# Performance work log

Hardware: AMD Instinct MI355X
Metric: run time of the kernel (lower is better)

## Reference

```python
import jax, jax.numpy as jnp
import numpy as np

B, L, D = 2, 4096, 1024
H, DK, DV = 4, 256, 256
CONV_K, FIR_S, FIR_L = 4, 3, 31
CHUNK = 32
EPS = 1e-5


def l2norm(x):
    return x * jax.lax.rsqrt(jnp.sum(x * x, -1, keepdims=True) + 1e-6)


def causal_dwconv(x, w):
    # x: [B, L, C], w: [C, K] depthwise causal FIR conv (left pad K-1)
    C, K = w.shape
    y = jax.lax.conv_general_dilated(
        jnp.swapaxes(x, 1, 2), w[:, None, :], (1,), [(K - 1, 0)],
        feature_group_count=C, dimension_numbers=('NCH', 'OIH', 'NCH'))
    return jnp.swapaxes(y, 1, 2)


def delta_rule_chunkwise(q, k, v, beta, chunk=CHUNK):
    # q,k: [b,h,L,dk], v: [b,h,L,dv], beta: [b,h,L]
    b, h, Lx, dk = q.shape
    dv = v.shape[-1]
    pad = (-Lx) % chunk
    if pad:
        q, k, v = (jnp.pad(t, ((0, 0), (0, 0), (0, pad), (0, 0))) for t in (q, k, v))
        beta = jnp.pad(beta, ((0, 0), (0, 0), (0, pad)))
    Lp = Lx + pad
    n = Lp // chunk
    q = l2norm(q)
    k = l2norm(k)
    v = v * beta[..., None]
    k_beta = k * beta[..., None]
    ch = lambda t: t.reshape(b, h, n, chunk, -1)
    qc, kc, vc, kbc = map(ch, (q, k, v, k_beta))
    # UT transform: T = (I + strictly_lower(k_beta @ k^T))^{-1}
    A = jnp.einsum('bhncd,bhned->bhnce', kbc, kc)
    eye = jnp.eye(chunk, dtype=q.dtype)
    T = jnp.linalg.inv(eye + jnp.tril(A, -1))  # same math as the sequential forward-substitution loop
    u = T @ vc      # [b,h,n,c,dv]
    w = T @ kbc     # [b,h,n,c,dk]
    tri = jnp.tril(jnp.ones((chunk, chunk), bool))  # causal incl. diagonal

    def body(S, inp):
        q_i, k_i, u_i, w_i = inp
        attn = jnp.where(tri, jnp.einsum('bhcd,bhed->bhce', q_i, k_i), 0.)
        u_i = u_i - w_i @ S
        o_i = q_i @ S + attn @ u_i
        S = S + jnp.einsum('bhcd,bhce->bhde', k_i, u_i)
        return S, o_i

    mv = lambda t: jnp.moveaxis(t, 2, 0)
    S0 = jnp.zeros((b, h, dk, dv), q.dtype)
    S, o = jax.lax.scan(body, S0, (mv(qc), mv(kc), mv(u), mv(w)))
    o = jnp.moveaxis(o, 0, 2).reshape(b, h, Lp, dv)[:, :, :Lx]
    return o, S


def setup_inputs() -> dict:
    key = jax.random.key(0)
    ks = jax.random.split(key, 16)
    s = 0.02
    fir_short = jnp.zeros((H, DV, FIR_S)).at[..., -1].set(1.0) + 1e-3 * jax.random.normal(ks[8], (H, DV, FIR_S))
    fir_long = jnp.zeros((H, DV, FIR_L)).at[..., -1].set(1.0) + 1e-3 * jax.random.normal(ks[9], (H, DV, FIR_L))
    bl = jnp.zeros((H, 3)).at[:, 0].set(2.0).reshape(-1)  # value_path_bias
    return dict(
        hidden_states=jax.random.normal(ks[0], (B, L, D), jnp.float32),
        Wq=s * jax.random.normal(ks[1], (D, H * DK)),
        Wk=s * jax.random.normal(ks[2], (D, H * DK)),
        Wv=s * jax.random.normal(ks[3], (D, H * DV)),
        conv_q=0.3 * jax.random.normal(ks[4], (H * DK, CONV_K)),
        conv_k=0.3 * jax.random.normal(ks[5], (H * DK, CONV_K)),
        conv_v=0.3 * jax.random.normal(ks[6], (H * DV, CONV_K)),
        Wb=s * jax.random.normal(ks[7], (D, H)),
        fir_short=fir_short,
        fir_long=fir_long,
        Wg=s * jax.random.normal(ks[10], (D, H)),
        bg=0.5 * jnp.ones((H,)),  # global_gate_bias
        Wl=s * jax.random.normal(ks[11], (D, H * 3)),
        bl=bl,
        log_temp=jnp.ones((H,)),  # log(e * temp_init) with temp_init=1
        rms_w=jnp.ones((DV,)),
        Wo=s * jax.random.normal(ks[12], (H * DV, D)),
    )


def reference(hidden_states, Wq, Wk, Wv, conv_q, conv_k, conv_v, Wb,
              fir_short, fir_long, Wg, bg, Wl, bl, log_temp, rms_w, Wo):
    x = hidden_states
    Bx, Lx, _ = x.shape
    # q/k/v projections + causal short conv + SiLU (qk_activation='silu')
    q = jax.nn.silu(causal_dwconv(x @ Wq, conv_q)).reshape(Bx, Lx, H, DK)
    k = jax.nn.silu(causal_dwconv(x @ Wk, conv_k)).reshape(Bx, Lx, H, DK)
    v = jax.nn.silu(causal_dwconv(x @ Wv, conv_v)).reshape(Bx, Lx, H, DV)
    beta = jax.nn.sigmoid(x @ Wb)  # [B,L,H]
    o_d, S = delta_rule_chunkwise(
        q.transpose(0, 2, 1, 3), k.transpose(0, 2, 1, 3),
        v.transpose(0, 2, 1, 3), beta.transpose(0, 2, 1))
    delta_out = o_d.transpose(0, 2, 1, 3)  # [B,L,H,DV]
    # local FIR paths on v (per-head depthwise causal FIR)
    vf = v.reshape(Bx, Lx, H * DV)
    local_short = causal_dwconv(vf, fir_short.reshape(H * DV, FIR_S)).reshape(Bx, Lx, H, DV)
    local_long = causal_dwconv(vf, fir_long.reshape(H * DV, FIR_L)).reshape(Bx, Lx, H, DV)
    # hierarchical two-stage gating with learnable per-head temperature
    w_global = jax.nn.sigmoid(x @ Wg + bg)  # [B,L,H]
    temp = jnp.exp(log_temp)                # [H]
    logits = (x @ Wl + bl).reshape(Bx, Lx, H, 3) / temp[:, None]
    p = jax.nn.softmax(logits, axis=-1)
    local_mix = p[..., 0:1] * v + p[..., 1:2] * local_short + p[..., 2:3] * local_long
    o = w_global[..., None] * delta_out + (1.0 - w_global)[..., None] * local_mix
    # per-head RMSNorm then output projection
    o = o * jax.lax.rsqrt(jnp.mean(o * o, -1, keepdims=True) + EPS) * rms_w
    return o.reshape(Bx, Lx, H * DV) @ Wo
```

## Files before the change

### kernel.cpp

```cpp
#include <hip/hip_runtime.h>
#include <hip/hip_bf16.h>
#include <math.h>

#define Bn 2
#define Ln 4096
#define Dn 1024
#define Hn 4
#define DKn 256
#define DVn 256
#define NCHn 128

typedef __attribute__((ext_vector_type(8))) short short8;
typedef __attribute__((ext_vector_type(4))) float f32x4;

__device__ __forceinline__ float sigmoidf_(float x) { return 1.f / (1.f + __expf(-x)); }

__device__ __forceinline__ unsigned short f2bf(float f) {
  union { float f; unsigned u; } v; v.f = f;
  unsigned r = v.u + 0x7FFFu + ((v.u >> 16) & 1u);
  return (unsigned short)(r >> 16);
}

__device__ __forceinline__ float bf2f(unsigned short u) {
  union { unsigned u; float f; } v; v.u = ((unsigned)u) << 16;
  return v.f;
}

__device__ __forceinline__ unsigned cvt_pk_bf16(float a, float b) {
  unsigned r;
  asm volatile("v_cvt_pk_bf16_f32 %0, %1, %2" : "=v"(r) : "v"(a), "v"(b));
  return r;
}

__device__ __forceinline__ short8 pack_i4(int4 o) {
  short8 r;
  __builtin_memcpy(&r, &o, 16);
  return r;
}

__device__ __forceinline__ void gl2lds16(const void* g, void* l) {
  __builtin_amdgcn_global_load_lds((const __attribute__((address_space(1))) unsigned int*)g,
                                   (__attribute__((address_space(3))) unsigned int*)l, 16, 0, 0);
}

__global__ __launch_bounds__(256) void wt_all_kernel(
    const float* __restrict__ W0, const float* __restrict__ W1,
    const float* __restrict__ W2, const float* __restrict__ W3,
    unsigned short* __restrict__ T0, unsigned short* __restrict__ T1,
    unsigned short* __restrict__ T2, unsigned short* __restrict__ T3) {
  const float* W = (blockIdx.z == 0) ? W0 : (blockIdx.z == 1) ? W1
                   : (blockIdx.z == 2) ? W2 : W3;
  unsigned short* Wt = (blockIdx.z == 0) ? T0 : (blockIdx.z == 1) ? T1
                       : (blockIdx.z == 2) ? T2 : T3;
  __shared__ float tile[32][33];
  const int bx = blockIdx.x * 32;
  const int by = blockIdx.y * 32;
  const int tx = threadIdx.x & 31, ty4 = (threadIdx.x >> 5) * 4;
#pragma unroll
  for (int r = 0; r < 4; ++r)
    tile[ty4 + r][tx] = W[(size_t)(by + ty4 + r) * 1024 + bx + tx];
  __syncthreads();
#pragma unroll
  for (int r = 0; r < 4; ++r)
    Wt[(size_t)(bx + ty4 + r) * 1024 + by + tx] = f2bf(tile[tx][ty4 + r]);
}

template <int OBF>
__global__ __launch_bounds__(256, 2) void gemm_bf16(const unsigned short* __restrict__ A,
                                                    const unsigned short* __restrict__ Bt,
                                                    void* __restrict__ Cv,
                                                    int M, int N, int K) {
  __shared__ __align__(16) unsigned short As[128 * 32];
  __shared__ __align__(16) unsigned short Bs[128 * 32];
  const int tid = threadIdx.x;
  const int wid = tid >> 6, lane = tid & 63;
  const int row0 = blockIdx.y * 128, col0 = blockIdx.x * 128;
  const int wr64 = (wid >> 1) * 64, wc64 = (wid & 1) * 64;
  const int fr = lane & 15, fg = lane >> 4;
  f32x4 acc[4][4];
#pragma unroll
  for (int i = 0; i < 4; ++i)
#pragma unroll
    for (int j = 0; j < 4; ++j) acc[i][j] = (f32x4){0.f, 0.f, 0.f, 0.f};
  for (int k0 = 0; k0 < K; k0 += 32) {
#pragma unroll
    for (int i = 0; i < 2; ++i) {
      const int off = wid * 2048 + i * 1024 + (lane << 4);
      const int r = off >> 6;
      const int kb = off & 63;
      gl2lds16((const char*)A + ((size_t)(row0 + r) * K + k0) * 2 + kb, (char*)As + off);
      gl2lds16((const char*)Bt + ((size_t)(col0 + r) * K + k0) * 2 + kb, (char*)Bs + off);
    }
    __syncthreads();
    short8 a[4], b[4];
#pragma unroll
    for (int mi = 0; mi < 4; ++mi)
      a[mi] = *(const short8*)&As[(wr64 + mi * 16 + fr) * 32 + fg * 8];
#pragma unroll
    for (int ni = 0; ni < 4; ++ni)
      b[ni] = *(const short8*)&Bs[(wc64 + ni * 16 + fr) * 32 + fg * 8];
#pragma unroll
    for (int mi = 0; mi < 4; ++mi)
#pragma unroll
      for (int ni = 0; ni < 4; ++ni)
        acc[mi][ni] = __builtin_amdgcn_mfma_f32_16x16x32_bf16(a[mi], b[ni], acc[mi][ni], 0, 0, 0);
    __syncthreads();
  }
#pragma unroll
  for (int mi = 0; mi < 4; ++mi) {
    const int orow = row0 + wr64 + mi * 16 + fg * 4;
#pragma unroll
    for (int ni = 0; ni < 4; ++ni) {
      const int ocol = col0 + wc64 + ni * 16 + fr;
      if (OBF) {
        unsigned short* C = (unsigned short*)Cv;
#pragma unroll
        for (int r = 0; r < 4; ++r)
          C[(size_t)(orow + r) * N + ocol] = f2bf(acc[mi][ni][r]);
      } else {
        float* C = (float*)Cv;
#pragma unroll
        for (int r = 0; r < 4; ++r)
          C[(size_t)(orow + r) * N + ocol] = acc[mi][ni][r];
      }
    }
  }
}

__global__ __launch_bounds__(256) void gates_kernel(
    const float* __restrict__ x, const float* __restrict__ Wb,
    const float* __restrict__ Wg, const float* __restrict__ bg,
    const float* __restrict__ Wl, const float* __restrict__ bl,
    const float* __restrict__ log_temp, float* __restrict__ beta,
    float* __restrict__ wgl, float* __restrict__ pmix,
    unsigned short* __restrict__ xb) {
  const int wave = threadIdx.x >> 6, lane = threadIdx.x & 63;
  const int row = (blockIdx.x << 2) + wave;
  if (row >= Bn * Ln) return;
  const float* xr = x + (size_t)row * Dn;
  float acc[20];
#pragma unroll
  for (int c = 0; c < 20; ++c) acc[c] = 0.f;
#pragma unroll
  for (int i = 0; i < 4; ++i) {
    const float4 xv = *(const float4*)&xr[(lane << 2) + (i << 8)];
    ushort4 ob;
    ob.x = f2bf(xv.x); ob.y = f2bf(xv.y); ob.z = f2bf(xv.z); ob.w = f2bf(xv.w);
    *(ushort4*)&xb[(size_t)row * Dn + (i << 8) + (lane << 2)] = ob;
    const float xa[4] = {xv.x, xv.y, xv.z, xv.w};
#pragma unroll
    for (int j = 0; j < 4; ++j) {
      const int kk = (i << 8) + (lane << 2) + j;
      const float xx = xa[j];
#pragma unroll
      for (int h = 0; h < 4; ++h) acc[h] = fmaf(xx, Wb[kk * 4 + h], acc[h]);
#pragma unroll
      for (int h = 0; h < 4; ++h) acc[4 + h] = fmaf(xx, Wg[kk * 4 + h], acc[4 + h]);
#pragma unroll
      for (int c = 0; c < 12; ++c) acc[8 + c] = fmaf(xx, Wl[kk * 12 + c], acc[8 + c]);
    }
  }
#pragma unroll
  for (int c = 0; c < 20; ++c)
    for (int off = 32; off; off >>= 1) acc[c] += __shfl_down(acc[c], off);
  if (lane == 0) {
    const int b = row >> 12, l = row & (Ln - 1);
#pragma unroll
    for (int h = 0; h < 4; ++h)
      beta[((size_t)(b * Hn + h) << 12) + l] = sigmoidf_(acc[h]);
#pragma unroll
    for (int h = 0; h < 4; ++h) wgl[row * 4 + h] = sigmoidf_(acc[4 + h] + bg[h]);
#pragma unroll
    for (int h = 0; h < 4; ++h) {
      const float it = 1.f / __expf(log_temp[h]);
      const float l0 = (acc[8 + h * 3 + 0] + bl[h * 3 + 0]) * it;
      const float l1 = (acc[8 + h * 3 + 1] + bl[h * 3 + 1]) * it;
      const float l2 = (acc[8 + h * 3 + 2] + bl[h * 3 + 2]) * it;
      const float mx = fmaxf(l0, fmaxf(l1, l2));
      const float e0 = __expf(l0 - mx), e1 = __expf(l1 - mx), e2 = __expf(l2 - mx);
      const float is = 1.f / (e0 + e1 + e2);
      pmix[row * 12 + h * 3 + 0] = e0 * is;
      pmix[row * 12 + h * 3 + 1] = e1 * is;
      pmix[row * 12 + h * 3 + 2] = e2 * is;
    }
  }
}

template <int DO_L2>
__global__ __launch_bounds__(256) void conv_act_kernel(
    const unsigned short* __restrict__ raw, const float* __restrict__ cw,
    unsigned short* __restrict__ out, int coloff) {
  const int blk = blockIdx.x;
  const int b = blk >> 12, l = blk & (Ln - 1);
  const int t = threadIdx.x;
  float vals[4];
#pragma unroll
  for (int g = 0; g < 4; ++g) {
    const int c = (g << 8) + t;
    float a = 0.f;
#pragma unroll
    for (int j = 0; j < 4; ++j) {
      const int ls = l - 3 + j;
      if (ls >= 0)
        a = fmaf(cw[c * 4 + j], bf2f(raw[(((size_t)b << 12) + ls) * 3072 + coloff + c]), a);
    }
    vals[g] = a * sigmoidf_(a);
  }
  if (DO_L2) {
    __shared__ float red[4][4];
    float ss[4];
#pragma unroll
    for (int g = 0; g < 4; ++g) ss[g] = vals[g] * vals[g];
#pragma unroll
    for (int g = 0; g < 4; ++g)
      for (int off = 32; off; off >>= 1) ss[g] += __shfl_down(ss[g], off);
    const int wave = t >> 6, lane = t & 63;
    if (lane == 0) {
#pragma unroll
      for (int g = 0; g < 4; ++g) red[wave][g] = ss[g];
    }
    __syncthreads();
#pragma unroll
    for (int g = 0; g < 4; ++g) {
      const float s = red[0][g] + red[1][g] + red[2][g] + red[3][g];
      vals[g] *= rsqrtf(s + 1e-6f);
    }
  }
#pragma unroll
  for (int g = 0; g < 4; ++g)
    out[((((size_t)(b * Hn + g)) << 12) + l) * 256 + t] = f2bf(vals[g]);
}

__global__ __launch_bounds__(256, 2) void precomp_kernel(
    const unsigned short* __restrict__ q, const unsigned short* __restrict__ k,
    const unsigned short* __restrict__ v, const float* __restrict__ beta,
    unsigned short* __restrict__ wfrag, unsigned short* __restrict__ qfrag,
    unsigned short* __restrict__ ktfrag, unsigned short* __restrict__ afrag,
    float* __restrict__ u0frag) {
  const int blk = blockIdx.x;
  const int n = blk & 127, bh = blk >> 7;
  const size_t base = (((size_t)bh << 12) + (n << 5)) * 256;
  const size_t cid = (size_t)(bh * NCHn + n);
  __shared__ __align__(16) unsigned short ksb[32][264];
  __shared__ __align__(16) unsigned short qsb[32][264];
  __shared__ __align__(16) unsigned short vbb[32][264];
  __shared__ float Tm[32][33], Am[32][33], bet[32];
  __shared__ __align__(16) float attn_l[32][36];
  const int t = threadIdx.x;
  const int wid = t >> 6, lane = t & 63;
  const int fr = lane & 15, fg = lane >> 4;
  if (t < 32) bet[t] = beta[((size_t)bh << 12) + (n << 5) + t];
#pragma unroll
  for (int it = 0; it < 4; ++it) {
    const int idx = t + it * 256;
    const int r = idx >> 5, c8 = (idx & 31) << 3;
    const float bv = beta[((size_t)bh << 12) + (n << 5) + r];
    *(int4*)&qsb[r][c8] = *(const int4*)&q[base + r * 256 + c8];
    *(int4*)&ksb[r][c8] = *(const int4*)&k[base + r * 256 + c8];
    const int4 vv = *(const int4*)&v[base + r * 256 + c8];
    const unsigned vu[4] = {(unsigned)vv.x, (unsigned)vv.y, (unsigned)vv.z, (unsigned)vv.w};
    int4 ov;
    ov.x = cvt_pk_bf16(bf2f((unsigned short)(vu[0] & 0xffff)) * bv,
                       bf2f((unsigned short)(vu[0] >> 16)) * bv);
    ov.y = cvt_pk_bf16(bf2f((unsigned short)(vu[1] & 0xffff)) * bv,
                       bf2f((unsigned short)(vu[1] >> 16)) * bv);
    ov.z = cvt_pk_bf16(bf2f((unsigned short)(vu[2] & 0xffff)) * bv,
                       bf2f((unsigned short)(vu[2] >> 16)) * bv);
    ov.w = cvt_pk_bf16(bf2f((unsigned short)(vu[3] & 0xffff)) * bv,
                       bf2f((unsigned short)(vu[3] >> 16)) * bv);
    *(int4*)&vbb[r][c8] = ov;
  }
  __syncthreads();
  {
    const int ti = wid >> 1, tj = wid & 1;
    f32x4 G = (f32x4){0.f, 0.f, 0.f, 0.f};
    f32x4 At = (f32x4){0.f, 0.f, 0.f, 0.f};
#pragma unroll
    for (int kw = 0; kw < 8; ++kw) {
      const short8 krow = *(const short8*)&ksb[ti * 16 + fr][kw * 32 + fg * 8];
      const short8 kcol = *(const short8*)&ksb[tj * 16 + fr][kw * 32 + fg * 8];
      const short8 qrow = *(const short8*)&qsb[ti * 16 + fr][kw * 32 + fg * 8];
      G = __builtin_amdgcn_mfma_f32_16x16x32_bf16(krow, kcol, G, 0, 0, 0);
      At = __builtin_amdgcn_mfma_f32_16x16x32_bf16(qrow, kcol, At, 0, 0, 0);
    }
#pragma unroll
    for (int r_ = 0; r_ < 4; ++r_) {
      const int i = ti * 16 + fg * 4 + r_;
      const int j = tj * 16 + fr;
      Am[i][j] = bet[i] * G[r_];
      attn_l[i][j] = (j <= i) ? At[r_] : 0.f;
    }
  }
#pragma unroll
  for (int it = 0; it < 4; ++it) {
    const int u = it * 4 + wid;
    const int mi = u >> 3, kw = u & 7;
    *(int4*)&qfrag[cid * 8192 + u * 512 + lane * 8] =
        *(const int4*)&qsb[mi * 16 + fr][kw * 32 + fg * 8];
  }
#pragma unroll
  for (int it = 0; it < 4; ++it) {
    const int mi = it * 4 + wid;
    const int dk = mi * 16 + fr;
    unsigned short e[8];
#pragma unroll
    for (int j = 0; j < 8; ++j) e[j] = ksb[fg * 8 + j][dk];
    int4 o;
    o.x = e[0] | ((unsigned)e[1] << 16);
    o.y = e[2] | ((unsigned)e[3] << 16);
    o.z = e[4] | ((unsigned)e[5] << 16);
    o.w = e[6] | ((unsigned)e[7] << 16);
    *(int4*)&ktfrag[cid * 8192 + mi * 512 + lane * 8] = o;
  }
  __syncthreads();
  if (t >= 128) {
    const int mi = (t >> 6) - 2;
    const int c = mi * 16 + fr;
    const float4 a = *(const float4*)&attn_l[c][fg * 8];
    const float4 b2 = *(const float4*)&attn_l[c][fg * 8 + 4];
    int4 o;
    o.x = f2bf(a.x) | ((unsigned)f2bf(a.y) << 16);
    o.y = f2bf(a.z) | ((unsigned)f2bf(a.w) << 16);
    o.z = f2bf(b2.x) | ((unsigned)f2bf(b2.y) << 16);
    o.w = f2bf(b2.z) | ((unsigned)f2bf(b2.w) << 16);
    *(int4*)&afrag[cid * 1024 + mi * 512 + lane * 8] = o;
  }
  if (t < 32) {
    float Tcol[32];
    Tcol[0] = (t == 0) ? 1.f : 0.f;
#pragma unroll
    for (int i = 1; i < 32; ++i) {
      float s0 = 0.f, s1 = 0.f;
      int m = 0;
#pragma unroll
      for (; m + 2 <= i; m += 2) {
        s0 = fmaf(Am[i][m], Tcol[m], s0);
        s1 = fmaf(Am[i][m + 1], Tcol[m + 1], s1);
      }
      if (m < i) s0 = fmaf(Am[i][m], Tcol[m], s0);
      Tcol[i] = ((i == t) ? 1.f : 0.f) - s0 - s1;
    }
#pragma unroll
    for (int i = 0; i < 32; ++i) Tm[i][t] = Tcol[i];
  }
  __syncthreads();
  {
    float betr[8];
#pragma unroll
    for (int j = 0; j < 8; ++j) betr[j] = bet[fg * 8 + j];
    short8 Tf[2], Tbf[2];
#pragma unroll
    for (int mi = 0; mi < 2; ++mi) {
      float tv[8];
#pragma unroll
      for (int j = 0; j < 8; ++j) tv[j] = Tm[mi * 16 + fr][fg * 8 + j];
      int4 p, pb;
      p.x = cvt_pk_bf16(tv[0], tv[1]); p.y = cvt_pk_bf16(tv[2], tv[3]);
      p.z = cvt_pk_bf16(tv[4], tv[5]); p.w = cvt_pk_bf16(tv[6], tv[7]);
      pb.x = cvt_pk_bf16(tv[0] * betr[0], tv[1] * betr[1]);
      pb.y = cvt_pk_bf16(tv[2] * betr[2], tv[3] * betr[3]);
      pb.z = cvt_pk_bf16(tv[4] * betr[4], tv[5] * betr[5]);
      pb.w = cvt_pk_bf16(tv[6] * betr[6], tv[7] * betr[7]);
      Tf[mi] = pack_i4(p);
      Tbf[mi] = pack_i4(pb);
    }
    const f32x4 zero = (f32x4){0.f, 0.f, 0.f, 0.f};
#pragma unroll
    for (int tt = 0; tt < 4; ++tt) {
      const int tjc = wid * 4 + tt;
      unsigned short ev[8], ek[8];
#pragma unroll
      for (int j = 0; j < 8; ++j) {
        ev[j] = vbb[fg * 8 + j][tjc * 16 + fr];
        ek[j] = ksb[fg * 8 + j][tjc * 16 + fr];
      }
      int4 pv, pk;
      pv.x = ev[0] | ((unsigned)ev[1] << 16); pv.y = ev[2] | ((unsigned)ev[3] << 16);
      pv.z = ev[4] | ((unsigned)ev[5] << 16); pv.w = ev[6] | ((unsigned)ev[7] << 16);
      pk.x = ek[0] | ((unsigned)ek[1] << 16); pk.y = ek[2] | ((unsigned)ek[3] << 16);
      pk.z = ek[4] | ((unsigned)ek[5] << 16); pk.w = ek[6] | ((unsigned)ek[7] << 16);
      const short8 vbf = pack_i4(pv);
      const short8 kbf = pack_i4(pk);
#pragma unroll
      for (int mi = 0; mi < 2; ++mi) {
        const f32x4 U = __builtin_amdgcn_mfma_f32_16x16x32_bf16(Tf[mi], vbf, zero, 0, 0, 0);
        *(f32x4*)&u0frag[cid * 8192 + (tjc * 2 + mi) * 256 + lane * 4] = U;
        const f32x4 W = __builtin_amdgcn_mfma_f32_16x16x32_bf16(Tbf[mi], kbf, zero, 0, 0, 0);
#pragma unroll
        for (int r_ = 0; r_ < 4; ++r_)
          qsb[mi * 16 + fg * 4 + r_][tjc * 16 + fr] = f2bf(W[r_]);
      }
    }
  }
  __syncthreads();
#pragma unroll
  for (int it = 0; it < 4; ++it) {
    const int u = it * 4 + wid;
    const int mi = u >> 3, kw = u & 7;
    *(int4*)&wfrag[cid * 8192 + u * 512 + lane * 8] =
        *(const int4*)&qsb[mi * 16 + fr][kw * 32 + fg * 8];
  }
}

__global__ __launch_bounds__(128, 1) void scan_mfma(
    const unsigned short* __restrict__ wfrag, const unsigned short* __restrict__ qfrag,
    const unsigned short* __restrict__ ktfrag, const unsigned short* __restrict__ afrag,
    const float* __restrict__ u0frag, unsigned short* __restrict__ dout) {
  const int bh = blockIdx.x & 7;
  const int dvs = blockIdx.x >> 3;
  const int tid = threadIdx.x;
  const int w = tid >> 6;
  const int lane = tid & 63;
  const int fr = lane & 15, fg = lane >> 4;
  const int swz = (fr & 7) << 4;
  __shared__ __align__(16) unsigned short St[2][2048];
  __shared__ __align__(16) unsigned short ut2[2][512];
  __shared__ __align__(16) float pux[2][2][2][256];
  __shared__ __align__(16) float pox[2][2][2][256];
  f32x4 S[8];
#pragma unroll
  for (int i = 0; i < 8; ++i) S[i] = (f32x4){0.f, 0.f, 0.f, 0.f};

  const unsigned short* wbase = wfrag + (size_t)(bh * NCHn) * 8192;
  const unsigned short* qbase = qfrag + (size_t)(bh * NCHn) * 8192;
  const unsigned short* kbase = ktfrag + (size_t)(bh * NCHn) * 8192;
  const unsigned short* abase = afrag + (size_t)(bh * NCHn) * 1024;
  const float* ubase = u0frag + (size_t)(bh * NCHn) * 8192 + dvs * 512;

  short8 wr[8], qr[8], ktr[8];
  short8 ar[2] = {};
  f32x4 u0r[2];
#pragma unroll
  for (int u8 = 0; u8 < 8; ++u8) {
    const int mi = u8 >> 2, kwp = u8 & 3;
    const int u = mi * 8 + 4 * w + kwp;
    wr[u8] = *(const short8*)&wbase[u * 512 + lane * 8];
    qr[u8] = *(const short8*)&qbase[u * 512 + lane * 8];
    ktr[u8] = *(const short8*)&kbase[(8 * w + u8) * 512 + lane * 8];
  }
#pragma unroll
  for (int u = 0; u < 2; ++u) u0r[u] = *(const f32x4*)&ubase[u * 256 + lane * 4];
  if (w == 0) {
#pragma unroll
    for (int u = 0; u < 2; ++u) ar[u] = *(const short8*)&abase[u * 512 + lane * 8];
  }

  for (int n = 0; n < NCHn; ++n) {
    const int np = (n + 1 < NCHn) ? (n + 1) : n;
    const int buf = n & 1;
#pragma unroll
    for (int mi = 0; mi < 8; ++mi) {
      const unsigned w0 = cvt_pk_bf16(S[mi][0], S[mi][1]);
      const unsigned w1 = cvt_pk_bf16(S[mi][2], S[mi][3]);
      const int a = (fr * 256 + mi * 32 + fg * 8) ^ swz;
      *(uint2*)((char*)&St[w][0] + a) = make_uint2(w0, w1);
    }
    short8 sb[4];
#pragma unroll
    for (int kwp = 0; kwp < 4; ++kwp) {
      const int a = (fr * 256 + kwp * 64 + fg * 16) ^ swz;
      sb[kwp] = *(const short8*)((const char*)&St[w][0] + a);
    }
    f32x4 up[2], oq[2];
    up[0] = up[1] = (f32x4){0.f, 0.f, 0.f, 0.f};
    oq[0] = oq[1] = (f32x4){0.f, 0.f, 0.f, 0.f};
#pragma unroll
    for (int kwp = 0; kwp < 4; ++kwp) {
#pragma unroll
      for (int mi = 0; mi < 2; ++mi) {
        up[mi] = __builtin_amdgcn_mfma_f32_16x16x32_bf16(wr[mi * 4 + kwp], sb[kwp], up[mi], 0, 0, 0);
        oq[mi] = __builtin_amdgcn_mfma_f32_16x16x32_bf16(qr[mi * 4 + kwp], sb[kwp], oq[mi], 0, 0, 0);
      }
    }
    {
      const unsigned short* wp = wbase + (size_t)np * 8192;
      const unsigned short* qp = qbase + (size_t)np * 8192;
#pragma unroll
      for (int u8 = 0; u8 < 8; ++u8) {
        const int mi = u8 >> 2, kwp = u8 & 3;
        const int u = mi * 8 + 4 * w + kwp;
        wr[u8] = *(const short8*)&wp[u * 512 + lane * 8];
        qr[u8] = *(const short8*)&qp[u * 512 + lane * 8];
      }
    }
#pragma unroll
    for (int mi = 0; mi < 2; ++mi) {
      *(f32x4*)&pux[w][buf][mi][lane * 4] = up[mi];
      *(f32x4*)&pox[w][buf][mi][lane * 4] = oq[mi];
    }
    asm volatile("s_waitcnt lgkmcnt(0)" ::: "memory");
    __builtin_amdgcn_s_barrier();
    __builtin_amdgcn_sched_barrier(0);
    f32x4 o_f[2];
#pragma unroll
    for (int mi = 0; mi < 2; ++mi) {
      const f32x4 puo = *(const f32x4*)&pux[w ^ 1][buf][mi][lane * 4];
      const f32x4 uu = u0r[mi] - up[mi] - puo;
      const unsigned a0 = cvt_pk_bf16(uu[0], uu[1]);
      const unsigned a1 = cvt_pk_bf16(uu[2], uu[3]);
      const int ad = (fr * 64 + mi * 32 + fg * 8) ^ swz;
      *(uint2*)((char*)&ut2[w][0] + ad) = make_uint2(a0, a1);
      o_f[mi] = oq[mi] + *(const f32x4*)&pox[w ^ 1][buf][mi][lane * 4];
    }
    asm volatile("s_waitcnt lgkmcnt(0)" ::: "memory");
    __builtin_amdgcn_sched_barrier(0);
    const short8 ub = *(const short8*)((const char*)&ut2[w][0] + ((fr * 64 + fg * 16) ^ swz));
    if (w == 0) {
#pragma unroll
      for (int mi = 0; mi < 2; ++mi)
        o_f[mi] = __builtin_amdgcn_mfma_f32_16x16x32_bf16(ar[mi], ub, o_f[mi], 0, 0, 0);
      const unsigned short* ap = abase + (size_t)np * 1024;
#pragma unroll
      for (int u = 0; u < 2; ++u) ar[u] = *(const short8*)&ap[u * 512 + lane * 8];
      const size_t cb = ((size_t)((bh << 12) + (n << 5))) * 256;
#pragma unroll
      for (int mi = 0; mi < 2; ++mi)
#pragma unroll
        for (int r = 0; r < 4; ++r)
          dout[cb + (size_t)(mi * 16 + fg * 4 + r) * 256 + dvs * 16 + fr] = f2bf(o_f[mi][r]);
    }
    {
      const float* up_ = ubase + (size_t)np * 8192;
#pragma unroll
      for (int u = 0; u < 2; ++u) u0r[u] = *(const f32x4*)&up_[u * 256 + lane * 4];
    }
#pragma unroll
    for (int mi = 0; mi < 8; ++mi)
      S[mi] = __builtin_amdgcn_mfma_f32_16x16x32_bf16(ktr[mi], ub, S[mi], 0, 0, 0);
    {
      const unsigned short* kp = kbase + (size_t)np * 8192;
#pragma unroll
      for (int u8 = 0; u8 < 8; ++u8)
        ktr[u8] = *(const short8*)&kp[(8 * w + u8) * 512 + lane * 8];
    }
  }
}

#define MIX_LT 16
__global__ __launch_bounds__(256) void mix_kernel(
    const unsigned short* __restrict__ v, const unsigned short* __restrict__ delta,
    const float* __restrict__ wgl, const float* __restrict__ pmix,
    const float* __restrict__ firs, const float* __restrict__ firl,
    const float* __restrict__ rms_w, unsigned short* __restrict__ out) {
  const int wgid = ((int)blockIdx.x & 7) * 256 + ((int)blockIdx.x >> 3);
  const int b = wgid >> 10;
  const int h = (wgid >> 8) & 3;
  const int lt = wgid & 255;
  const int l0 = lt * MIX_LT;
  const int t = threadIdx.x;
  const int wv = t >> 6, lane = t & 63;
  const unsigned short* vcol = v + ((((size_t)(b * Hn + h)) << 12)) * 256 + t;
  const unsigned short* dcol = delta + ((((size_t)(b * Hn + h)) << 12)) * 256 + t;
  float fw[31], fs3[3];
#pragma unroll
  for (int j = 0; j < 31; ++j) fw[j] = firl[((h << 8) + t) * 31 + j];
#pragma unroll
  for (int j = 0; j < 3; ++j) fs3[j] = firs[((h << 8) + t) * 3 + j];
  const float rw = rms_w[t];
  float vbuf[46];
#pragma unroll
  for (int j = 0; j < 30; ++j) {
    const int ls = l0 - 30 + j;
    vbuf[j] = (ls >= 0) ? bf2f(vcol[(size_t)ls * 256]) : 0.f;
  }
#pragma unroll
  for (int i = 0; i < MIX_LT; ++i) vbuf[30 + i] = bf2f(vcol[(size_t)(l0 + i) * 256]);
  __shared__ float wred[MIX_LT * 4];
  float o[MIX_LT];
#pragma unroll
  for (int i = 0; i < MIX_LT; ++i) {
    const int l = l0 + i;
    const float vnew = vbuf[30 + i];
    float lo = fw[30] * vnew;
#pragma unroll
    for (int j = 0; j < 30; ++j) lo = fmaf(fw[j], vbuf[i + j], lo);
    float sh = fs3[2] * vnew;
    sh = fmaf(fs3[1], vbuf[i + 29], sh);
    sh = fmaf(fs3[0], vbuf[i + 28], sh);
    const int row = (b << 12) + l;
    const float p0 = pmix[row * 12 + h * 3 + 0];
    const float p1 = pmix[row * 12 + h * 3 + 1];
    const float p2 = pmix[row * 12 + h * 3 + 2];
    const float wg = wgl[row * 4 + h];
    const float mixv = p0 * vnew + p1 * sh + p2 * lo;
    const float oo = wg * bf2f(dcol[(size_t)l * 256]) + (1.f - wg) * mixv;
    o[i] = oo;
    float ss = oo * oo;
#pragma unroll
    for (int m = 1; m < 64; m <<= 1) ss += __shfl_xor(ss, m);
    if (lane == 0) wred[i * 4 + wv] = ss;
  }
  __syncthreads();
#pragma unroll
  for (int i = 0; i < MIX_LT; ++i) {
    const float sum = wred[i * 4] + wred[i * 4 + 1] + wred[i * 4 + 2] + wred[i * 4 + 3];
    const float sc = rsqrtf(sum * (1.f / 256.f) + 1e-5f);
    const int l = l0 + i;
    out[(size_t)((b << 12) + l) * 1024 + (h << 8) + t] = f2bf(o[i] * sc * rw);
  }
}

extern "C" void kernel_launch(void* const* d_in, const int* in_sizes, int n_in,
                              void* d_out, int out_size, void* d_ws, size_t ws_size,
                              hipStream_t stream) {
  const float* x = (const float*)d_in[0];
  const float* Wq = (const float*)d_in[1];
  const float* Wk = (const float*)d_in[2];
  const float* Wv = (const float*)d_in[3];
  const float* cq = (const float*)d_in[4];
  const float* ck = (const float*)d_in[5];
  const float* cv = (const float*)d_in[6];
  const float* Wb = (const float*)d_in[7];
  const float* firs = (const float*)d_in[8];
  const float* firl = (const float*)d_in[9];
  const float* Wg = (const float*)d_in[10];
  const float* bg = (const float*)d_in[11];
  const float* Wl = (const float*)d_in[12];
  const float* bl = (const float*)d_in[13];
  const float* ltemp = (const float*)d_in[14];
  const float* rmsw = (const float*)d_in[15];
  const float* Wo = (const float*)d_in[16];

  float* ws = (float*)d_ws;
  const size_t NE = (size_t)Bn * Ln * 1024;
  unsigned short* qkvbf = (unsigned short*)ws;
  unsigned short* wfrag = (unsigned short*)ws;
  unsigned short* qfrag = wfrag + 8388608;
  unsigned short* ktfrag = (unsigned short*)(ws + NE);
  unsigned short* afrag = ktfrag + 8388608;
  float* u0frag = ws + 2 * NE;
  unsigned short* xb = (unsigned short*)(ws + 3 * NE);
  unsigned short* normed_bf = xb;
  unsigned short* Wqt = xb + NE;
  unsigned short* Wkt = Wqt + 1048576;
  unsigned short* Wvt = Wkt + 1048576;
  unsigned short* qn_bf = (unsigned short*)(ws + 4 * NE);
  unsigned short* kn_bf = qn_bf + NE;
  unsigned short* vn_bf = (unsigned short*)(ws + 5 * NE);
  unsigned short* dout_bf = vn_bf + NE;
  float* beta = ws + 6 * NE;
  float* wgl = beta + (size_t)Bn * Hn * Ln;
  float* pmix = wgl + (size_t)Bn * Ln * Hn;
  unsigned short* Wot = (unsigned short*)(pmix + (size_t)Bn * Ln * Hn * 3);

  wt_all_kernel<<<dim3(32, 32, 4), 256, 0, stream>>>(Wq, Wk, Wv, Wo,
                                                     Wqt, Wkt, Wvt, Wot);
  gates_kernel<<<Bn * Ln / 4, 256, 0, stream>>>(x, Wb, Wg, bg, Wl, bl, ltemp,
                                                beta, wgl, pmix, xb);
  gemm_bf16<1><<<dim3(24, 64), 256, 0, stream>>>(xb, Wqt, qkvbf, Bn * Ln, 3072, 1024);
  conv_act_kernel<1><<<Bn * Ln, 256, 0, stream>>>(qkvbf, cq, qn_bf, 0);
  conv_act_kernel<1><<<Bn * Ln, 256, 0, stream>>>(qkvbf, ck, kn_bf, 1024);
  conv_act_kernel<0><<<Bn * Ln, 256, 0, stream>>>(qkvbf, cv, vn_bf, 2048);
  precomp_kernel<<<Bn * Hn * NCHn, 256, 0, stream>>>(qn_bf, kn_bf, vn_bf, beta,
                                                     wfrag, qfrag, ktfrag, afrag,
                                                     u0frag);
  scan_mfma<<<128, 128, 0, stream>>>(wfrag, qfrag, ktfrag, afrag, u0frag, dout_bf);
  mix_kernel<<<Bn * Hn * (Ln / MIX_LT), 256, 0, stream>>>(
      vn_bf, dout_bf, wgl, pmix, firs, firl, rmsw, normed_bf);
  gemm_bf16<0><<<dim3(8, 64), 256, 0, stream>>>(normed_bf, Wot, (float*)d_out,
                                                Bn * Ln, 1024, 1024);
}
```

Before: 444.6 us.

## Fuse q/k/v causal conv kernels into one sliding-window tile kernel

Replaces three per-row conv+SiLU(+L2norm) launches with a single kernel in which each block handles 16 consecutive positions for q, k and v together. The 3-tap history is kept in registers as a sliding window, so each input element is read once instead of four times, and the filter weights are loaded once per block instead of once per row. In exchange the grid shrinks to 512 blocks, and each position step now ends in block-wide barriers for the shared-memory reduction, which may limit occupancy and parallelism.

```diff
diff --git a/kernel.cpp b/kernel.cpp
--- a/kernel.cpp
+++ b/kernel.cpp
@@ -186,49 +186,105 @@
   }
 }
 
-template <int DO_L2>
-__global__ __launch_bounds__(256) void conv_act_kernel(
-    const unsigned short* __restrict__ raw, const float* __restrict__ cw,
-    unsigned short* __restrict__ out, int coloff) {
-  const int blk = blockIdx.x;
-  const int b = blk >> 12, l = blk & (Ln - 1);
+#define CLT 16
+__global__ __launch_bounds__(256) void conv_fused_kernel(
+    const unsigned short* __restrict__ qkv, const float* __restrict__ cq,
+    const float* __restrict__ ck, const float* __restrict__ cv,
+    unsigned short* __restrict__ qn, unsigned short* __restrict__ kn,
+    unsigned short* __restrict__ vn) {
+  const int wgid = ((int)blockIdx.x & 7) * 64 + ((int)blockIdx.x >> 3);
+  const int b = wgid >> 8;
+  const int lt = wgid & 255;
+  const int l0 = lt * CLT;
   const int t = threadIdx.x;
-  float vals[4];
-#pragma unroll
-  for (int g = 0; g < 4; ++g) {
-    const int c = (g << 8) + t;
-    float a = 0.f;
+  const int wv = t >> 6, lane = t & 63;
+  float wq[4][4], wk[4][4], wvw[4][4];
+#pragma unroll
+  for (int g = 0; g < 4; ++g)
 #pragma unroll
     for (int j = 0; j < 4; ++j) {
-      const int ls = l - 3 + j;
-      if (ls >= 0)
-        a = fmaf(cw[c * 4 + j], bf2f(raw[(((size_t)b << 12) + ls) * 3072 + coloff + c]), a);
-    }
-    vals[g] = a * sigmoidf_(a);
-  }
-  if (DO_L2) {
-    __shared__ float red[4][4];
-    float ss[4];
-#pragma unroll
-    for (int g = 0; g < 4; ++g) ss[g] = vals[g] * vals[g];
-#pragma unroll
-    for (int g = 0; g < 4; ++g)
-      for (int off = 32; off; off >>= 1) ss[g] += __shfl_down(ss[g], off);
-    const int wave = t >> 6, lane = t & 63;
+      wq[g][j] = cq[((g << 8) + t) * 4 + j];
+      wk[g][j] = ck[((g << 8) + t) * 4 + j];
+      wvw[g][j] = cv[((g << 8) + t) * 4 + j];
+    }
+  float hq[4][3], hk[4][3], hv[4][3];
+#pragma unroll
+  for (int jj = 0; jj < 3; ++jj) {
+    const int ls = l0 - 3 + jj;
+    if (ls >= 0) {
+      const size_t rb = (((size_t)b << 12) + ls) * 3072;
+#pragma unroll
+      for (int g = 0; g < 4; ++g) {
+        hq[g][jj] = bf2f(qkv[rb + (g << 8) + t]);
+        hk[g][jj] = bf2f(qkv[rb + 1024 + (g << 8) + t]);
+        hv[g][jj] = bf2f(qkv[rb + 2048 + (g << 8) + t]);
+      }
+    } else {
+#pragma unroll
+      for (int g = 0; g < 4; ++g) { hq[g][jj] = 0.f; hk[g][jj] = 0.f; hv[g][jj] = 0.f; }
+    }
+  }
+  __shared__ float red[4][8];
+#pragma unroll
+  for (int i = 0; i < CLT; ++i) {
+    const int l = l0 + i;
+    const size_t rb = (((size_t)b << 12) + l) * 3072;
+    float cq_[4], ck_[4], cv_[4];
+#pragma unroll
+    for (int g = 0; g < 4; ++g) {
+      cq_[g] = bf2f(qkv[rb + (g << 8) + t]);
+      ck_[g] = bf2f(qkv[rb + 1024 + (g << 8) + t]);
+      cv_[g] = bf2f(qkv[rb + 2048 + (g << 8) + t]);
+    }
+    float aq[4], ak[4], av[4];
+#pragma unroll
+    for (int g = 0; g < 4; ++g) {
+      float a = wq[g][3] * cq_[g];
+      a = fmaf(wq[g][0], hq[g][0], a);
+      a = fmaf(wq[g][1], hq[g][1], a);
+      a = fmaf(wq[g][2], hq[g][2], a);
+      aq[g] = a * sigmoidf_(a);
+      float bkv = wk[g][3] * ck_[g];
+      bkv = fmaf(wk[g][0], hk[g][0], bkv);
+      bkv = fmaf(wk[g][1], hk[g][1], bkv);
+      bkv = fmaf(wk[g][2], hk[g][2], bkv);
+      ak[g] = bkv * sigmoidf_(bkv);
+      float c = wvw[g][3] * cv_[g];
+      c = fmaf(wvw[g][0], hv[g][0], c);
+      c = fmaf(wvw[g][1], hv[g][1], c);
+      c = fmaf(wvw[g][2], hv[g][2], c);
+      av[g] = c * sigmoidf_(c);
+      hq[g][0] = hq[g][1]; hq[g][1] = hq[g][2]; hq[g][2] = cq_[g];
+      hk[g][0] = hk[g][1]; hk[g][1] = hk[g][2]; hk[g][2] = ck_[g];
+      hv[g][0] = hv[g][1]; hv[g][1] = hv[g][2]; hv[g][2] = cv_[g];
+    }
+    float sq[4], sk[4];
+#pragma unroll
+    for (int g = 0; g < 4; ++g) { sq[g] = aq[g] * aq[g]; sk[g] = ak[g] * ak[g]; }
+#pragma unroll
+    for (int m = 1; m < 64; m <<= 1) {
+#pragma unroll
+      for (int g = 0; g < 4; ++g) {
+        sq[g] += __shfl_xor(sq[g], m);
+        sk[g] += __shfl_xor(sk[g], m);
+      }
+    }
     if (lane == 0) {
 #pragma unroll
-      for (int g = 0; g < 4; ++g) red[wave][g] = ss[g];
+      for (int g = 0; g < 4; ++g) { red[wv][g] = sq[g]; red[wv][4 + g] = sk[g]; }
     }
     __syncthreads();
 #pragma unroll
     for (int g = 0; g < 4; ++g) {
-      const float s = red[0][g] + red[1][g] + red[2][g] + red[3][g];
-      vals[g] *= rsqrtf(s + 1e-6f);
-    }
-  }
-#pragma unroll
-  for (int g = 0; g < 4; ++g)
-    out[((((size_t)(b * Hn + g)) << 12) + l) * 256 + t] = f2bf(vals[g]);
+      const float rq = rsqrtf(red[0][g] + red[1][g] + red[2][g] + red[3][g] + 1e-6f);
+      const float rk = rsqrtf(red[0][4 + g] + red[1][4 + g] + red[2][4 + g] + red[3][4 + g] + 1e-6f);
+      const size_t ob = ((((size_t)(b * Hn + g)) << 12) + l) * 256 + t;
+      qn[ob] = f2bf(aq[g] * rq);
+      kn[ob] = f2bf(ak[g] * rk);
+      vn[ob] = f2bf(av[g]);
+    }
+    __syncthreads();
+  }
 }
 
 __global__ __launch_bounds__(256, 2) void precomp_kernel(
@@ -648,9 +704,8 @@
   gates_kernel<<<Bn * Ln / 4, 256, 0, stream>>>(x, Wb, Wg, bg, Wl, bl, ltemp,
                                                 beta, wgl, pmix, xb);
   gemm_bf16<1><<<dim3(24, 64), 256, 0, stream>>>(xb, Wqt, qkvbf, Bn * Ln, 3072, 1024);
-  conv_act_kernel<1><<<Bn * Ln, 256, 0, stream>>>(qkvbf, cq, qn_bf, 0);
-  conv_act_kernel<1><<<Bn * Ln, 256, 0, stream>>>(qkvbf, ck, kn_bf, 1024);
-  conv_act_kernel<0><<<Bn * Ln, 256, 0, stream>>>(qkvbf, cv, vn_bf, 2048);
+  conv_fused_kernel<<<Bn * (Ln / CLT), 256, 0, stream>>>(qkvbf, cq, ck, cv,
+                                                         qn_bf, kn_bf, vn_bf);
   precomp_kernel<<<Bn * Hn * NCHn, 256, 0, stream>>>(qn_bf, kn_bf, vn_bf, beta,
                                                      wfrag, qfrag, ktfrag, afrag,
                                                      u0frag);
```

After: 469.5 us. +5.6%, slower.

## Fuse q/k/v causal conv+SiLU+L2 into one sequence-tiled vectorized kernel

Applied to the files above, without the earlier changes.

Replaces three per-position conv_act launches with a single kernel. Each block handles 16 consecutive positions for all three tensors, with 8 channels per thread loaded as 16-byte vectors. A register sliding window reuses the previous three inputs, so each input is read about once instead of four times. The per-head L2 norm becomes a 32-lane xor shuffle with no shared memory or barrier. This cuts launch count, redundant global reads and scalar loads, but gives fewer, larger blocks (512 blocks of 384 threads) and a serial loop per thread.

```diff
diff --git a/kernel.cpp b/kernel.cpp
--- a/kernel.cpp
+++ b/kernel.cpp
@@ -186,49 +186,80 @@
   }
 }
 
-template <int DO_L2>
-__global__ __launch_bounds__(256) void conv_act_kernel(
-    const unsigned short* __restrict__ raw, const float* __restrict__ cw,
-    unsigned short* __restrict__ out, int coloff) {
-  const int blk = blockIdx.x;
-  const int b = blk >> 12, l = blk & (Ln - 1);
+#define CLT 16
+__global__ __launch_bounds__(384) void conv_fused_kernel(
+    const unsigned short* __restrict__ qkv, const float* __restrict__ cq,
+    const float* __restrict__ ck, const float* __restrict__ cv,
+    unsigned short* __restrict__ qn, unsigned short* __restrict__ kn,
+    unsigned short* __restrict__ vn) {
+  const int wgid = ((int)blockIdx.x & 7) * 64 + ((int)blockIdx.x >> 3);
+  const int b = wgid >> 8;
+  const int lt = wgid & 255;
+  const int l0 = lt * CLT;
   const int t = threadIdx.x;
-  float vals[4];
-#pragma unroll
-  for (int g = 0; g < 4; ++g) {
-    const int c = (g << 8) + t;
-    float a = 0.f;
-#pragma unroll
-    for (int j = 0; j < 4; ++j) {
-      const int ls = l - 3 + j;
-      if (ls >= 0)
-        a = fmaf(cw[c * 4 + j], bf2f(raw[(((size_t)b << 12) + ls) * 3072 + coloff + c]), a);
-    }
-    vals[g] = a * sigmoidf_(a);
-  }
-  if (DO_L2) {
-    __shared__ float red[4][4];
-    float ss[4];
-#pragma unroll
-    for (int g = 0; g < 4; ++g) ss[g] = vals[g] * vals[g];
-#pragma unroll
-    for (int g = 0; g < 4; ++g)
-      for (int off = 32; off; off >>= 1) ss[g] += __shfl_down(ss[g], off);
-    const int wave = t >> 6, lane = t & 63;
-    if (lane == 0) {
-#pragma unroll
-      for (int g = 0; g < 4; ++g) red[wave][g] = ss[g];
-    }
-    __syncthreads();
-#pragma unroll
-    for (int g = 0; g < 4; ++g) {
-      const float s = red[0][g] + red[1][g] + red[2][g] + red[3][g];
-      vals[g] *= rsqrtf(s + 1e-6f);
-    }
-  }
-#pragma unroll
-  for (int g = 0; g < 4; ++g)
-    out[((((size_t)(b * Hn + g)) << 12) + l) * 256 + t] = f2bf(vals[g]);
+  const int tensor = t >> 7;
+  const int head = (t & 127) >> 5;
+  const int ch0 = (t & 31) * 8;
+  const int col = tensor * 1024 + head * 256 + ch0;
+  const float* cw = (tensor == 0) ? cq : (tensor == 1) ? ck : cv;
+  float w4[8][4];
+#pragma unroll
+  for (int e = 0; e < 8; ++e)
+#pragma unroll
+    for (int j = 0; j < 4; ++j) w4[e][j] = cw[(head * 256 + ch0 + e) * 4 + j];
+  float h0[8], h1[8], h2[8];
+#pragma unroll
+  for (int e = 0; e < 8; ++e) { h0[e] = 0.f; h1[e] = 0.f; h2[e] = 0.f; }
+  {
+    const int ls0 = l0 - 3;
+    if (ls0 >= 0) {
+      const short8 r = *(const short8*)&qkv[(((size_t)b << 12) + ls0) * 3072 + col];
+#pragma unroll
+      for (int e = 0; e < 8; ++e) h0[e] = bf2f((unsigned short)r[e]);
+    }
+    if (l0 - 2 >= 0) {
+      const short8 r = *(const short8*)&qkv[(((size_t)b << 12) + l0 - 2) * 3072 + col];
+#pragma unroll
+      for (int e = 0; e < 8; ++e) h1[e] = bf2f((unsigned short)r[e]);
+    }
+    if (l0 - 1 >= 0) {
+      const short8 r = *(const short8*)&qkv[(((size_t)b << 12) + l0 - 1) * 3072 + col];
+#pragma unroll
+      for (int e = 0; e < 8; ++e) h2[e] = bf2f((unsigned short)r[e]);
+    }
+  }
+  unsigned short* outp = (tensor == 0) ? qn : (tensor == 1) ? kn : vn;
+  const size_t obase = (((size_t)(b * Hn + head)) << 12) * 256 + ch0;
+#pragma unroll
+  for (int i = 0; i < CLT; ++i) {
+    const int l = l0 + i;
+    const short8 r = *(const short8*)&qkv[(((size_t)b << 12) + l) * 3072 + col];
+    float cur[8], a[8];
+#pragma unroll
+    for (int e = 0; e < 8; ++e) cur[e] = bf2f((unsigned short)r[e]);
+    float ssq = 0.f;
+#pragma unroll
+    for (int e = 0; e < 8; ++e) {
+      float s = w4[e][3] * cur[e];
+      s = fmaf(w4[e][0], h0[e], s);
+      s = fmaf(w4[e][1], h1[e], s);
+      s = fmaf(w4[e][2], h2[e], s);
+      const float y = s * sigmoidf_(s);
+      a[e] = y;
+      ssq = fmaf(y, y, ssq);
+      h0[e] = h1[e]; h1[e] = h2[e]; h2[e] = cur[e];
+    }
+    float sc = 1.f;
+    if (tensor < 2) {
+#pragma unroll
+      for (int m = 1; m <= 16; m <<= 1) ssq += __shfl_xor(ssq, m);
+      sc = rsqrtf(ssq + 1e-6f);
+    }
+    short8 o;
+#pragma unroll
+    for (int e = 0; e < 8; ++e) o[e] = (short)f2bf(a[e] * sc);
+    *(short8*)&outp[obase + (size_t)l * 256] = o;
+  }
 }
 
 __global__ __launch_bounds__(256, 2) void precomp_kernel(
@@ -648,9 +679,8 @@
   gates_kernel<<<Bn * Ln / 4, 256, 0, stream>>>(x, Wb, Wg, bg, Wl, bl, ltemp,
                                                 beta, wgl, pmix, xb);
   gemm_bf16<1><<<dim3(24, 64), 256, 0, stream>>>(xb, Wqt, qkvbf, Bn * Ln, 3072, 1024);
-  conv_act_kernel<1><<<Bn * Ln, 256, 0, stream>>>(qkvbf, cq, qn_bf, 0);
-  conv_act_kernel<1><<<Bn * Ln, 256, 0, stream>>>(qkvbf, ck, kn_bf, 1024);
-  conv_act_kernel<0><<<Bn * Ln, 256, 0, stream>>>(qkvbf, cv, vn_bf, 2048);
+  conv_fused_kernel<<<Bn * (Ln / CLT), 384, 0, stream>>>(qkvbf, cq, ck, cv,
+                                                         qn_bf, kn_bf, vn_bf);
   precomp_kernel<<<Bn * Hn * NCHn, 256, 0, stream>>>(qn_bf, kn_bf, vn_bf, beta,
                                                      wfrag, qfrag, ktfrag, afrag,
                                                      u0frag);
```

Result: faster. 372.3 us (-16.3%).
